# Kernel tuning notes

Hardware: AMD Instinct MI355X
Metric: run time of the kernel (lower is better)

Reference implementation:

```python
import jax, jax.numpy as jnp
import numpy as np
from jax import lax

K_NN = 3
LN_EPS = 1e-5


def _encode(x, W1, b1, W2, b2, W3, b3, gamma, beta):
    h = jax.nn.relu(x @ W1 + b1)
    h = jax.nn.relu(h @ W2 + b2)
    z = h @ W3 + b3
    mu = jnp.mean(z, axis=-1, keepdims=True)
    var = jnp.mean((z - mu) ** 2, axis=-1, keepdims=True)  # biased var, as torch LayerNorm
    return (z - mu) / jnp.sqrt(var + LN_EPS) * gamma + beta


def _state_entropy(src, tgt, k):
    # pairwise L2 distance via GEMM formulation (same math as torch.norm of diffs)
    sq = (jnp.sum(src * src, -1)[:, None]
          + jnp.sum(tgt * tgt, -1)[None, :]
          - 2.0 * (src @ tgt.T))
    dists = jnp.sqrt(jnp.maximum(sq, 0.0))  # [N_src, N_tgt]
    # sum of k smallest distances (kthvalue 1..k), single fused top-k
    neg_k, _ = lax.top_k(-dists, k)
    knn = jnp.sum(-neg_k, axis=-1)
    # faithful to the source bug: loop variable shadows k, final divisor is k-1
    knn = knn / float(k - 1)
    return knn[:, None]


def setup_inputs() -> dict:
    key = jax.random.key(0)
    ks = jax.random.split(key, 6)
    N, D, H, L = 16384, 128, 256, 256
    return {
        "state_src": jax.random.normal(ks[0], (N, D), jnp.float32),
        "state_tgt": jax.random.normal(ks[1], (N, D), jnp.float32),
        "W1": jax.random.normal(ks[2], (D, H), jnp.float32) * 0.05,
        "b1": jnp.zeros((H,), jnp.float32),
        "W2": jax.random.normal(ks[3], (H, H), jnp.float32) * 0.05,
        "b2": jnp.zeros((H,), jnp.float32),
        "W3": jax.random.normal(ks[4], (H, L), jnp.float32) * 0.05,
        "b3": jnp.zeros((L,), jnp.float32),
        "gamma": jnp.ones((L,), jnp.float32),
        "beta": jnp.zeros((L,), jnp.float32),
    }


def reference(state_src, state_tgt, W1, b1, W2, b2, W3, b3, gamma, beta):
    src = _encode(state_src, W1, b1, W2, b2, W3, b3, gamma, beta)  # forward()
    tgt = _encode(state_tgt, W1, b1, W2, b2, W3, b3, gamma, beta)
    entropy = _state_entropy(src, tgt, K_NN)  # compute_state_entropy (no_grad)
    return src, entropy
```

## Files before the change

kernel.cpp:

```cpp
#include <hip/hip_runtime.h>
#include <math.h>


typedef __attribute__((ext_vector_type(8))) short short8;
typedef __attribute__((ext_vector_type(4))) float floatx4;
typedef __attribute__((ext_vector_type(8))) int int8v;
typedef __attribute__((ext_vector_type(4))) int int4v;

#define MFMA16(a, b, c) __builtin_amdgcn_mfma_f32_16x16x32_bf16((a), (b), (c), 0, 0, 0)

__device__ __forceinline__ floatx4 mfma8(int8v a, int8v b, floatx4 c) {
  return __builtin_amdgcn_mfma_scale_f32_16x16x128_f8f6f4(a, b, c, 0, 0, 0, 0x7F, 0, 0x7F);
}

__device__ __forceinline__ int8v cat8(int4v lo, int4v hi) {
  return __builtin_shufflevector(lo, hi, 0, 1, 2, 3, 4, 5, 6, 7);
}

static const size_t OFF_W1F  = 0;
static const size_t OFF_W2F  = 65536;
static const size_t OFF_W3F  = 196608;
static const size_t OFF_SRCF = 327680;
static const size_t OFF_TGTF = 327680 + 8388608;
static const size_t OFF_S2   = 327680 + 2 * 8388608;
static const size_t OFF_T2   = OFF_S2 + 65536;
static const size_t OFF_P    = OFF_T2 + 65536;
static const size_t OFF_SRC8 = 18808832;
static const size_t OFF_TGT8 = 18808832 + 4194304;
static const size_t WS_NEED  = OFF_TGT8 + 4194304;

__device__ __forceinline__ unsigned short f2bf(float f) {
  unsigned int u = __float_as_uint(f);
  return (unsigned short)((u + 0x7FFFu + ((u >> 16) & 1u)) >> 16);
}

__device__ __forceinline__ unsigned int pkbf(float lo, float hi) {
  unsigned int r;
  asm("v_cvt_pk_bf16_f32 %0, %1, %2" : "=v"(r) : "v"(lo), "v"(hi));
  return r;
}

__device__ __forceinline__ void ins3(float& t0, float& t1, float& t2, float v) {
  float n0 = fminf(t0, v);
  float n1 = __builtin_amdgcn_fmed3f(t0, t1, v);
  float n2 = __builtin_amdgcn_fmed3f(t1, t2, v);
  t0 = n0; t1 = n1; t2 = n2;
}

__device__ __forceinline__ void gload16(const void* g, void* l) {
  __builtin_amdgcn_global_load_lds(
      (const __attribute__((address_space(1))) unsigned int*)(unsigned long long)(uintptr_t)g,
      (__attribute__((address_space(3))) unsigned int*)(unsigned int)(uintptr_t)l, 16, 0, 0);
}

__device__ __forceinline__ unsigned int sxor(unsigned int v, int m) {
  return (unsigned int)__shfl_xor((int)v, m, 64);
}

__device__ __forceinline__ void exchange8(const unsigned int* p0, const unsigned int* p1,
                                          short8* frag, int g) {
  const bool go = (g & 1), gh = (g >> 1);
#pragma unroll
  for (int ks = 0; ks < 8; ++ks) {
    unsigned int a_o = p0[2 * ks], b_o = p1[2 * ks];
    unsigned int c_o = p0[2 * ks + 1], d_o = p1[2 * ks + 1];
    unsigned int a_n = sxor(a_o, 16), b_n = sxor(b_o, 16);
    unsigned int c_n = sxor(c_o, 16), d_n = sxor(d_o, 16);
    unsigned int qab0 = go ? a_n : a_o, qab1 = go ? b_n : b_o;
    unsigned int qab2 = go ? a_o : a_n, qab3 = go ? b_o : b_n;
    unsigned int qcd0 = go ? c_n : c_o, qcd1 = go ? d_n : d_o;
    unsigned int qcd2 = go ? c_o : c_n, qcd3 = go ? d_o : d_n;
    unsigned int s0 = gh ? qab0 : qcd0, s1 = gh ? qab1 : qcd1;
    unsigned int s2 = gh ? qab2 : qcd2, s3 = gh ? qab3 : qcd3;
    unsigned int r0 = sxor(s0, 32), r1 = sxor(s1, 32);
    unsigned int r2 = sxor(s2, 32), r3 = sxor(s3, 32);
    union { unsigned int u[4]; short8 s; } cv;
    cv.u[0] = (g == 0) ? qab0 : (g == 3) ? qcd0 : r0;
    cv.u[1] = (g == 0) ? qab1 : (g == 3) ? qcd1 : r1;
    cv.u[2] = (g == 0) ? qab2 : (g == 3) ? qcd2 : r2;
    cv.u[3] = (g == 0) ? qab3 : (g == 3) ? qcd3 : r3;
    frag[ks] = cv.s;
  }
}

__global__ void prep_weights(const float* __restrict__ W1, const float* __restrict__ W2,
                             const float* __restrict__ W3, unsigned short* __restrict__ ws16) {
  int t = blockIdx.x * 256 + threadIdx.x;
  const float* W;
  unsigned short* dst;
  int f, ksbits;
  if (t < 4096)       { W = W1; dst = ws16 + OFF_W1F / 2; f = t;         ksbits = 2; }
  else if (t < 12288) { W = W2; dst = ws16 + OFF_W2F / 2; f = t - 4096;  ksbits = 3; }
  else                { W = W3; dst = ws16 + OFF_W3F / 2; f = t - 12288; ksbits = 3; }
  int l  = f & 63;
  int fk = f >> 6;
  int ks = fk & ((1 << ksbits) - 1);
  int cf = fk >> ksbits;
  int k0 = ks * 32 + ((l >> 4) << 3);
  int c  = (cf << 4) + (l & 15);
  short8 v;
#pragma unroll
  for (int j = 0; j < 8; ++j) v[j] = (short)f2bf(W[(size_t)(k0 + j) * 256 + c]);
  *(short8*)(dst + (size_t)f * 8) = v;
}

__global__ __launch_bounds__(256, 2) void encode_kernel(
    const float* __restrict__ xsrc, const float* __restrict__ xtgt,
    const float* __restrict__ b1, const float* __restrict__ b2, const float* __restrict__ b3,
    const float* __restrict__ gamma, const float* __restrict__ beta,
    float* __restrict__ out_src, unsigned short* __restrict__ ws16) {
  __shared__ unsigned short wlds[2][16384];
  const int tid = threadIdx.x, w = tid >> 6, l = tid & 63;
  const int dr = l & 15, g = l >> 4;
  const int blk = blockIdx.x;
  const bool is_src = blk < 256;
  const int row0 = ((blk & 255) << 6) + (w << 4);
  const int row = row0 + dr;
  const float* __restrict__ X = is_src ? xsrc : xtgt;
  unsigned short* __restrict__ fragout = ws16 + (is_src ? OFF_SRCF / 2 : OFF_TGTF / 2);
  float* __restrict__ nrm = (float*)(ws16 + (is_src ? OFF_S2 / 2 : OFF_T2 / 2));
  const unsigned short* W1f = ws16 + OFF_W1F / 2;
  const unsigned short* W2f = ws16 + OFF_W2F / 2;
  const unsigned short* W3f = ws16 + OFF_W3F / 2;

  auto stageW = [&](int bsel, int q) {
    const unsigned short* src;
    int rounds;
    if (q < 4)      { src = W1f + q * 8192;        rounds = 4; }
    else if (q < 8) { src = W2f + (q - 4) * 16384; rounds = 8; }
    else            { src = W3f + (q - 8) * 16384; rounds = 8; }
#pragma unroll
    for (int r = 0; r < 8; ++r) {
      if (r < rounds)
        gload16(src + r * 2048 + w * 512 + l * 8, &wlds[bsel][r * 2048 + w * 512]);
    }
  };

  short8 xf[4];
  const float* xr = X + (size_t)row * 128;
#pragma unroll
  for (int ks = 0; ks < 4; ++ks) {
    floatx4 f0 = *(const floatx4*)(xr + ks * 32 + g * 8);
    floatx4 f1 = *(const floatx4*)(xr + ks * 32 + g * 8 + 4);
    union { unsigned int u[4]; short8 s; } cv;
    cv.u[0] = pkbf(f0[0], f0[1]); cv.u[1] = pkbf(f0[2], f0[3]);
    cv.u[2] = pkbf(f1[0], f1[1]); cv.u[3] = pkbf(f1[2], f1[3]);
    xf[ks] = cv.s;
  }

  unsigned int p0[16], p1[16];
  short8 hf[8];

  stageW(0, 0);
  __syncthreads();
  int cur = 0;

#pragma unroll
  for (int qq = 0; qq < 4; ++qq) {
    stageW(cur ^ 1, qq + 1);
#pragma unroll
    for (int i = 0; i < 4; ++i) {
      int cf = qq * 4 + i;
      floatx4 acc = {0.f, 0.f, 0.f, 0.f};
#pragma unroll
      for (int ks = 0; ks < 4; ++ks) {
        short8 wf = *(const short8*)(&wlds[cur][((i * 4 + ks) * 64 + l) * 8]);
        acc = MFMA16(wf, xf[ks], acc);
      }
      floatx4 bv = *(const floatx4*)(b1 + cf * 16 + g * 4);
      float h0 = fmaxf(acc[0] + bv[0], 0.f), h1v = fmaxf(acc[1] + bv[1], 0.f);
      float h2v = fmaxf(acc[2] + bv[2], 0.f), h3v = fmaxf(acc[3] + bv[3], 0.f);
      p0[cf] = pkbf(h0, h1v); p1[cf] = pkbf(h2v, h3v);
    }
    __syncthreads();
    cur ^= 1;
  }
  exchange8(p0, p1, hf, g);

#pragma unroll
  for (int qq = 0; qq < 4; ++qq) {
    stageW(cur ^ 1, 5 + qq);
#pragma unroll
    for (int i = 0; i < 4; ++i) {
      int cf = qq * 4 + i;
      floatx4 acc = {0.f, 0.f, 0.f, 0.f};
#pragma unroll
      for (int ks = 0; ks < 8; ++ks) {
        short8 wf = *(const short8*)(&wlds[cur][((i * 8 + ks) * 64 + l) * 8]);
        acc = MFMA16(wf, hf[ks], acc);
      }
      floatx4 bv = *(const floatx4*)(b2 + cf * 16 + g * 4);
      float h0 = fmaxf(acc[0] + bv[0], 0.f), h1v = fmaxf(acc[1] + bv[1], 0.f);
      float h2v = fmaxf(acc[2] + bv[2], 0.f), h3v = fmaxf(acc[3] + bv[3], 0.f);
      p0[cf] = pkbf(h0, h1v); p1[cf] = pkbf(h2v, h3v);
    }
    __syncthreads();
    cur ^= 1;
  }
  exchange8(p0, p1, hf, g);

  floatx4 z[16];
#pragma unroll
  for (int qq = 0; qq < 4; ++qq) {
    if (qq < 3) stageW(cur ^ 1, 9 + qq);
#pragma unroll
    for (int i = 0; i < 4; ++i) {
      int cf = qq * 4 + i;
      floatx4 acc = {0.f, 0.f, 0.f, 0.f};
#pragma unroll
      for (int ks = 0; ks < 8; ++ks) {
        short8 wf = *(const short8*)(&wlds[cur][((i * 8 + ks) * 64 + l) * 8]);
        acc = MFMA16(wf, hf[ks], acc);
      }
      floatx4 bv = *(const floatx4*)(b3 + cf * 16 + g * 4);
#pragma unroll
      for (int j = 0; j < 4; ++j) acc[j] += bv[j];
      z[cf] = acc;
    }
    __syncthreads();
    cur ^= 1;
  }

  float s = 0.f, q = 0.f;
#pragma unroll
  for (int cf = 0; cf < 16; ++cf)
#pragma unroll
    for (int j = 0; j < 4; ++j) { float v = z[cf][j]; s += v; q = fmaf(v, v, q); }
  s += __shfl_xor(s, 16, 64); s += __shfl_xor(s, 32, 64);
  q += __shfl_xor(q, 16, 64); q += __shfl_xor(q, 32, 64);
  float mu = s * 0.00390625f;
  float var = q * 0.00390625f - mu * mu;
  float rstd = rsqrtf(var + 1e-5f);

  const float sc = is_src ? -2.0f : 1.0f;
  float nacc = 0.f;
#pragma unroll
  for (int cf = 0; cf < 16; ++cf) {
    floatx4 gv = *(const floatx4*)(gamma + cf * 16 + g * 4);
    floatx4 bev = *(const floatx4*)(beta + cf * 16 + g * 4);
    float y0 = (z[cf][0] - mu) * rstd * gv[0] + bev[0];
    float y1 = (z[cf][1] - mu) * rstd * gv[1] + bev[1];
    float y2 = (z[cf][2] - mu) * rstd * gv[2] + bev[2];
    float y3 = (z[cf][3] - mu) * rstd * gv[3] + bev[3];
    nacc = fmaf(y0, y0, nacc); nacc = fmaf(y1, y1, nacc);
    nacc = fmaf(y2, y2, nacc); nacc = fmaf(y3, y3, nacc);
    p0[cf] = pkbf(sc * y0, sc * y1); p1[cf] = pkbf(sc * y2, sc * y3);
  }
  nacc += __shfl_xor(nacc, 16, 64); nacc += __shfl_xor(nacc, 32, 64);
  if (g == 0) nrm[row] = nacc;

  short8 yf[8];
  exchange8(p0, p1, yf, g);

  const int tile = row0 >> 4;
#pragma unroll
  for (int ks = 0; ks < 8; ++ks)
    *(short8*)(fragout + ((size_t)(tile * 8 + ks) * 64 + l) * 8) = yf[ks];

  if (is_src) {
    float* orow = out_src + (size_t)row * 256;
#pragma unroll
    for (int ks = 0; ks < 8; ++ks) {
      union { short8 s; unsigned int u[4]; } cv; cv.s = yf[ks];
      floatx4 o0, o1;
      o0[0] = __uint_as_float(cv.u[0] << 16) * -0.5f;
      o0[1] = __uint_as_float(cv.u[0] & 0xffff0000u) * -0.5f;
      o0[2] = __uint_as_float(cv.u[1] << 16) * -0.5f;
      o0[3] = __uint_as_float(cv.u[1] & 0xffff0000u) * -0.5f;
      o1[0] = __uint_as_float(cv.u[2] << 16) * -0.5f;
      o1[1] = __uint_as_float(cv.u[2] & 0xffff0000u) * -0.5f;
      o1[2] = __uint_as_float(cv.u[3] << 16) * -0.5f;
      o1[3] = __uint_as_float(cv.u[3] & 0xffff0000u) * -0.5f;
      *(floatx4*)(orow + ks * 32 + g * 8) = o0;
      *(floatx4*)(orow + ks * 32 + g * 8 + 4) = o1;
    }
  }
}

__global__ __launch_bounds__(256) void repack_fp8(const unsigned short* __restrict__ ws16,
                                                  unsigned char* __restrict__ wsb) {
  int t = blockIdx.x * 256 + threadIdx.x;
  const int side = t >> 17;
  const int u = t & 131071;
  const int df = u >> 6, l = u & 63;
  const int tile = df >> 1, ks2 = df & 1;
  const unsigned short* sbase = ws16 + (side ? OFF_TGTF / 2 : OFF_SRCF / 2);
  unsigned char* dbase = wsb + (side ? OFF_TGT8 : OFF_SRC8);
  int r[8];
#pragma unroll
  for (int sub = 0; sub < 4; ++sub) {
    int sf = (tile * 8 + ks2 * 4 + (l >> 4)) * 64 + sub * 16 + (l & 15);
    short8 v = *(const short8*)(sbase + (size_t)sf * 8);
    float f[8];
#pragma unroll
    for (int j = 0; j < 8; ++j)
      f[j] = __uint_as_float(((unsigned int)(unsigned short)v[j]) << 16);
    unsigned int w0 = __builtin_amdgcn_cvt_pk_fp8_f32(f[0], f[1], 0, 0);
    w0 = __builtin_amdgcn_cvt_pk_fp8_f32(f[2], f[3], w0, 1);
    unsigned int w1 = __builtin_amdgcn_cvt_pk_fp8_f32(f[4], f[5], 0, 0);
    w1 = __builtin_amdgcn_cvt_pk_fp8_f32(f[6], f[7], w1, 1);
    r[sub * 2] = (int)w0;
    r[sub * 2 + 1] = (int)w1;
  }
  int4v rlo = {r[0], r[1], r[2], r[3]};
  int4v rhi = {r[4], r[5], r[6], r[7]};
  *(int4v*)(dbase + (size_t)df * 2048 + l * 16) = rlo;
  *(int4v*)(dbase + (size_t)df * 2048 + 1024 + l * 16) = rhi;
}

__global__ __launch_bounds__(256, 2) void dist8_kernel(
    const unsigned char* __restrict__ src8, const unsigned char* __restrict__ tgt8,
    const float* __restrict__ t2, float* __restrict__ part) {
  __shared__ unsigned char buf[2][32768];
  __shared__ float t2l[2048];
  const int tid = threadIdx.x, w = tid >> 6, l = tid & 63;
  const int blk = blockIdx.x;
  const int split = blk & 7;
  const int rtile = blk >> 3;
  const int R0 = rtile * 256 + w * 64;
  const int C0 = split * 2048;

  {
    floatx4 v0 = *(const floatx4*)(t2 + C0 + tid * 8);
    floatx4 v1 = *(const floatx4*)(t2 + C0 + tid * 8 + 4);
    *(floatx4*)(t2l + tid * 8) = v0;
    *(floatx4*)(t2l + tid * 8 + 4) = v1;
  }

  int8v a[4][2];
#pragma unroll
  for (int rf = 0; rf < 4; ++rf)
#pragma unroll
    for (int ks2 = 0; ks2 < 2; ++ks2) {
      const unsigned char* ab = src8 + ((size_t)((R0 >> 4) + rf) * 2 + ks2) * 2048;
      int4v lo = *(const int4v*)(ab + l * 16);
      int4v hi = *(const int4v*)(ab + 1024 + l * 16);
      a[rf][ks2] = cat8(lo, hi);
    }

  float t3[4][4][3];
#pragma unroll
  for (int rf = 0; rf < 4; ++rf)
#pragma unroll
    for (int j = 0; j < 4; ++j) { t3[rf][j][0] = 1e30f; t3[rf][j][1] = 1e30f; t3[rf][j][2] = 1e30f; }

  const unsigned char* gb0 = tgt8 + (size_t)(C0 >> 4) * 4096;
#define STAGE(bsel, t)                                                        \
  {                                                                           \
    const unsigned char* gb = gb0 + (size_t)(t) * 32768;                      \
    _Pragma("unroll") for (int i = 0; i < 8; ++i) {                           \
      int chunk = w * 8 + i;                                                  \
      gload16(gb + chunk * 1024 + l * 16, &buf[bsel][chunk * 1024]);          \
    }                                                                         \
  }

  STAGE(0, 0);
  __syncthreads();

  for (int t = 0; t < 16; ++t) {
    int cur = t & 1;
    if (t < 15) STAGE(cur ^ 1, t + 1);
#pragma unroll
    for (int cf = 0; cf < 8; ++cf) {
      const unsigned char* bb = &buf[cur][cf * 4096];
      int4v l0 = *(const int4v*)(bb + l * 16);
      int4v h0 = *(const int4v*)(bb + 1024 + l * 16);
      int4v l1 = *(const int4v*)(bb + 2048 + l * 16);
      int4v h1 = *(const int4v*)(bb + 3072 + l * 16);
      int8v b0 = cat8(l0, h0), b1 = cat8(l1, h1);
      float tv = t2l[t * 128 + cf * 16 + (l & 15)];
      floatx4 acc[4];
#pragma unroll
      for (int rf = 0; rf < 4; ++rf) acc[rf] = (floatx4){tv, tv, tv, tv};
      __builtin_amdgcn_s_setprio(1);
#pragma unroll
      for (int rf = 0; rf < 4; ++rf) acc[rf] = mfma8(a[rf][0], b0, acc[rf]);
#pragma unroll
      for (int rf = 0; rf < 4; ++rf) acc[rf] = mfma8(a[rf][1], b1, acc[rf]);
      __builtin_amdgcn_s_setprio(0);
#pragma unroll
      for (int rf = 0; rf < 4; ++rf)
#pragma unroll
        for (int j = 0; j < 4; ++j)
          ins3(t3[rf][j][0], t3[rf][j][1], t3[rf][j][2], acc[rf][j]);
    }
    __syncthreads();
  }
#undef STAGE

#pragma unroll
  for (int rf = 0; rf < 4; ++rf)
#pragma unroll
    for (int j = 0; j < 4; ++j)
#pragma unroll
      for (int m = 1; m < 16; m <<= 1) {
        float o0 = __shfl_xor(t3[rf][j][0], m, 64);
        float o1 = __shfl_xor(t3[rf][j][1], m, 64);
        float o2 = __shfl_xor(t3[rf][j][2], m, 64);
        ins3(t3[rf][j][0], t3[rf][j][1], t3[rf][j][2], o0);
        ins3(t3[rf][j][0], t3[rf][j][1], t3[rf][j][2], o1);
        ins3(t3[rf][j][0], t3[rf][j][1], t3[rf][j][2], o2);
      }
  if ((l & 15) == 0) {
    int q = l >> 4;
#pragma unroll
    for (int rf = 0; rf < 4; ++rf)
#pragma unroll
      for (int j = 0; j < 4; ++j) {
        int row = R0 + rf * 16 + q * 4 + j;
        float* p = part + ((size_t)row * 8 + split) * 3;
        p[0] = t3[rf][j][0];
        p[1] = t3[rf][j][1];
        p[2] = t3[rf][j][2];
      }
  }
}

__global__ __launch_bounds__(512, 2) void dist_kernel(
    const unsigned short* __restrict__ srcf, const unsigned short* __restrict__ tgtf,
    const float* __restrict__ t2, float* __restrict__ part) {
  __shared__ unsigned short buf[2][32768];
  const int tid = threadIdx.x, w = tid >> 6, l = tid & 63;
  const int blk = blockIdx.x;
  const int split = blk & 7;
  const int rtile = blk >> 3;
  const int R0 = rtile * 512 + w * 64;
  const int C0 = split * 2048;

  short8 a[4][8];
#pragma unroll
  for (int rf = 0; rf < 4; ++rf)
#pragma unroll
    for (int ks = 0; ks < 8; ++ks)
      a[rf][ks] = *(const short8*)(srcf + (((size_t)(R0 / 16 + rf) * 8 + ks) * 64 + l) * 8);

  float t3[4][4][3];
#pragma unroll
  for (int rf = 0; rf < 4; ++rf)
#pragma unroll
    for (int j = 0; j < 4; ++j) { t3[rf][j][0] = 1e30f; t3[rf][j][1] = 1e30f; t3[rf][j][2] = 1e30f; }

  const unsigned short* gb0 = tgtf + (size_t)(C0 / 16) * 4096;
#define STAGE(bsel, t)                                                        \
  {                                                                           \
    const unsigned short* gb = gb0 + (size_t)(t) * 32768;                     \
    _Pragma("unroll") for (int i = 0; i < 8; ++i) {                           \
      int chunk = w * 8 + i;                                                  \
      gload16(gb + chunk * 512 + l * 8, &buf[bsel][chunk * 512]);             \
    }                                                                         \
  }

  STAGE(0, 0);
  float t2v[8];
#pragma unroll
  for (int c = 0; c < 8; ++c) t2v[c] = t2[C0 + c * 16 + (l & 15)];
  __syncthreads();

  for (int t = 0; t < 16; ++t) {
    int cur = t & 1;
    if (t < 15) STAGE(cur ^ 1, t + 1);
    float t2n[8];
    if (t < 15) {
      int nb = C0 + (t + 1) * 128;
#pragma unroll
      for (int c = 0; c < 8; ++c) t2n[c] = t2[nb + c * 16 + (l & 15)];
    }
#pragma unroll
    for (int cf = 0; cf < 8; ++cf) {
      const unsigned short* bb = &buf[cur][cf << 12];
      float tv = t2v[cf];
      floatx4 acc[4];
      short8 bc = *(const short8*)(bb + l * 8);
#pragma unroll
      for (int rf = 0; rf < 4; ++rf) acc[rf] = (floatx4){tv, tv, tv, tv};
      __builtin_amdgcn_s_setprio(1);
#pragma unroll
      for (int ks = 0; ks < 8; ++ks) {
        short8 bn = bc;
        if (ks < 7) bn = *(const short8*)(bb + (ks + 1) * 512 + l * 8);
#pragma unroll
        for (int rf = 0; rf < 4; ++rf) acc[rf] = MFMA16(a[rf][ks], bc, acc[rf]);
        bc = bn;
      }
      __builtin_amdgcn_s_setprio(0);
#pragma unroll
      for (int rf = 0; rf < 4; ++rf)
#pragma unroll
        for (int j = 0; j < 4; ++j)
          ins3(t3[rf][j][0], t3[rf][j][1], t3[rf][j][2], acc[rf][j]);
    }
#pragma unroll
    for (int c = 0; c < 8; ++c) t2v[c] = t2n[c];
    __syncthreads();
  }
#undef STAGE

#pragma unroll
  for (int rf = 0; rf < 4; ++rf)
#pragma unroll
    for (int j = 0; j < 4; ++j)
#pragma unroll
      for (int m = 1; m < 16; m <<= 1) {
        float o0 = __shfl_xor(t3[rf][j][0], m, 64);
        float o1 = __shfl_xor(t3[rf][j][1], m, 64);
        float o2 = __shfl_xor(t3[rf][j][2], m, 64);
        ins3(t3[rf][j][0], t3[rf][j][1], t3[rf][j][2], o0);
        ins3(t3[rf][j][0], t3[rf][j][1], t3[rf][j][2], o1);
        ins3(t3[rf][j][0], t3[rf][j][1], t3[rf][j][2], o2);
      }
  if ((l & 15) == 0) {
    int q = l >> 4;
#pragma unroll
    for (int rf = 0; rf < 4; ++rf)
#pragma unroll
      for (int j = 0; j < 4; ++j) {
        int row = R0 + rf * 16 + q * 4 + j;
        float* p = part + ((size_t)row * 8 + split) * 3;
        p[0] = t3[rf][j][0];
        p[1] = t3[rf][j][1];
        p[2] = t3[rf][j][2];
      }
  }
}

__global__ void merge_kernel(const float* __restrict__ part, const float* __restrict__ s2,
                             float* __restrict__ eout) {
  int r = blockIdx.x * 256 + threadIdx.x;
  const float* p = part + (size_t)r * 24;
  float u0 = 1e30f, u1 = 1e30f, u2 = 1e30f;
#pragma unroll
  for (int i = 0; i < 24; ++i) ins3(u0, u1, u2, p[i]);
  float sv = s2[r];
  float d0 = sqrtf(fmaxf(sv + u0, 0.f));
  float d1 = sqrtf(fmaxf(sv + u1, 0.f));
  float d2 = sqrtf(fmaxf(sv + u2, 0.f));
  eout[r] = (d0 + d1 + d2) * 0.5f;
}

extern "C" void kernel_launch(void* const* d_in, const int* in_sizes, int n_in,
                              void* d_out, int out_size, void* d_ws, size_t ws_size,
                              hipStream_t stream) {
  const float* xsrc = (const float*)d_in[0];
  const float* xtgt = (const float*)d_in[1];
  const float* W1 = (const float*)d_in[2];
  const float* b1 = (const float*)d_in[3];
  const float* W2 = (const float*)d_in[4];
  const float* b2 = (const float*)d_in[5];
  const float* W3 = (const float*)d_in[6];
  const float* b3 = (const float*)d_in[7];
  const float* gm = (const float*)d_in[8];
  const float* bt = (const float*)d_in[9];
  float* out = (float*)d_out;
  unsigned short* ws16 = (unsigned short*)d_ws;
  unsigned char* wsb = (unsigned char*)d_ws;

  prep_weights<<<80, 256, 0, stream>>>(W1, W2, W3, ws16);
  encode_kernel<<<512, 256, 0, stream>>>(xsrc, xtgt, b1, b2, b3, gm, bt, out, ws16);
  if (ws_size >= WS_NEED) {
    repack_fp8<<<1024, 256, 0, stream>>>(ws16, wsb);
    dist8_kernel<<<512, 256, 0, stream>>>(wsb + OFF_SRC8, wsb + OFF_TGT8,
                                          (const float*)(wsb + OFF_T2),
                                          (float*)(wsb + OFF_P));
  } else {
    dist_kernel<<<256, 512, 0, stream>>>(ws16 + OFF_SRCF / 2, ws16 + OFF_TGTF / 2,
                                         (const float*)(wsb + OFF_T2),
                                         (float*)(wsb + OFF_P));
  }
  merge_kernel<<<64, 256, 0, stream>>>((const float*)(wsb + OFF_P),
                                       (const float*)(wsb + OFF_S2),
                                       out + 4194304);
}
```

Measured before the change: 120.5 us.

## Load FP8 target tiles directly from global into registers, dropping LDS staging

The distance kernel no longer stages target fp8 tiles and squared norms through double-buffered shared memory with block barriers. Each wave now reads B fragments and norm values straight from global memory into registers, using a two-deep register ping-pong to prefetch the next column chunk. This removes LDS traffic, __syncthreads and the shared memory footprint, which could raise occupancy. The cost is that all four waves read the same target data separately, relying on L2/L1 hits, and global load latency is now hidden by only one chunk of lookahead.

```diff
diff --git a/kernel.cpp b/kernel.cpp
--- a/kernel.cpp
+++ b/kernel.cpp
@@ -308,24 +308,15 @@
   *(int4v*)(dbase + (size_t)df * 2048 + 1024 + l * 16) = rhi;
 }
 
-__global__ __launch_bounds__(256, 2) void dist8_kernel(
+__global__ __launch_bounds__(256, 2) void dist9_kernel(
     const unsigned char* __restrict__ src8, const unsigned char* __restrict__ tgt8,
     const float* __restrict__ t2, float* __restrict__ part) {
-  __shared__ unsigned char buf[2][32768];
-  __shared__ float t2l[2048];
   const int tid = threadIdx.x, w = tid >> 6, l = tid & 63;
   const int blk = blockIdx.x;
   const int split = blk & 7;
-  const int rtile = blk >> 3;
-  const int R0 = rtile * 256 + w * 64;
+  const int rg = (blk >> 3) * 4 + w;
+  const int R0 = rg * 64;
   const int C0 = split * 2048;
-
-  {
-    floatx4 v0 = *(const floatx4*)(t2 + C0 + tid * 8);
-    floatx4 v1 = *(const floatx4*)(t2 + C0 + tid * 8 + 4);
-    *(floatx4*)(t2l + tid * 8) = v0;
-    *(floatx4*)(t2l + tid * 8 + 4) = v1;
-  }
 
   int8v a[4][2];
 #pragma unroll
@@ -344,49 +335,48 @@
 #pragma unroll
     for (int j = 0; j < 4; ++j) { t3[rf][j][0] = 1e30f; t3[rf][j][1] = 1e30f; t3[rf][j][2] = 1e30f; }
 
-  const unsigned char* gb0 = tgt8 + (size_t)(C0 >> 4) * 4096;
-#define STAGE(bsel, t)                                                        \
+  const unsigned char* bb = tgt8 + (size_t)(C0 >> 4) * 4096 + l * 16;
+  const float* t2g = t2 + C0;
+
+#define LOADB(c, x0, x1, x2, x3, tv)                                          \
   {                                                                           \
-    const unsigned char* gb = gb0 + (size_t)(t) * 32768;                      \
-    _Pragma("unroll") for (int i = 0; i < 8; ++i) {                           \
-      int chunk = w * 8 + i;                                                  \
-      gload16(gb + chunk * 1024 + l * 16, &buf[bsel][chunk * 1024]);          \
-    }                                                                         \
-  }
-
-  STAGE(0, 0);
-  __syncthreads();
-
-  for (int t = 0; t < 16; ++t) {
-    int cur = t & 1;
-    if (t < 15) STAGE(cur ^ 1, t + 1);
-#pragma unroll
-    for (int cf = 0; cf < 8; ++cf) {
-      const unsigned char* bb = &buf[cur][cf * 4096];
-      int4v l0 = *(const int4v*)(bb + l * 16);
-      int4v h0 = *(const int4v*)(bb + 1024 + l * 16);
-      int4v l1 = *(const int4v*)(bb + 2048 + l * 16);
-      int4v h1 = *(const int4v*)(bb + 3072 + l * 16);
-      int8v b0 = cat8(l0, h0), b1 = cat8(l1, h1);
-      float tv = t2l[t * 128 + cf * 16 + (l & 15)];
-      floatx4 acc[4];
-#pragma unroll
-      for (int rf = 0; rf < 4; ++rf) acc[rf] = (floatx4){tv, tv, tv, tv};
-      __builtin_amdgcn_s_setprio(1);
-#pragma unroll
-      for (int rf = 0; rf < 4; ++rf) acc[rf] = mfma8(a[rf][0], b0, acc[rf]);
-#pragma unroll
-      for (int rf = 0; rf < 4; ++rf) acc[rf] = mfma8(a[rf][1], b1, acc[rf]);
-      __builtin_amdgcn_s_setprio(0);
-#pragma unroll
-      for (int rf = 0; rf < 4; ++rf)
-#pragma unroll
-        for (int j = 0; j < 4; ++j)
-          ins3(t3[rf][j][0], t3[rf][j][1], t3[rf][j][2], acc[rf][j]);
-    }
-    __syncthreads();
-  }
-#undef STAGE
+    const unsigned char* p = bb + (size_t)(c) * 4096;                         \
+    x0 = *(const int4v*)(p);                                                  \
+    x1 = *(const int4v*)(p + 1024);                                           \
+    x2 = *(const int4v*)(p + 2048);                                           \
+    x3 = *(const int4v*)(p + 3072);                                           \
+    tv = t2g[(c) * 16 + (l & 15)];                                            \
+  }
+
+#define COMPB(x0, x1, x2, x3, tv)                                             \
+  {                                                                           \
+    int8v b0 = cat8(x0, x1), b1 = cat8(x2, x3);                               \
+    floatx4 acc[4];                                                           \
+    _Pragma("unroll") for (int rf = 0; rf < 4; ++rf)                          \
+        acc[rf] = (floatx4){tv, tv, tv, tv};                                  \
+    __builtin_amdgcn_s_setprio(1);                                            \
+    _Pragma("unroll") for (int rf = 0; rf < 4; ++rf)                          \
+        acc[rf] = mfma8(a[rf][0], b0, acc[rf]);                               \
+    _Pragma("unroll") for (int rf = 0; rf < 4; ++rf)                          \
+        acc[rf] = mfma8(a[rf][1], b1, acc[rf]);                               \
+    __builtin_amdgcn_s_setprio(0);                                            \
+    _Pragma("unroll") for (int rf = 0; rf < 4; ++rf)                          \
+      _Pragma("unroll") for (int j = 0; j < 4; ++j)                           \
+          ins3(t3[rf][j][0], t3[rf][j][1], t3[rf][j][2], acc[rf][j]);         \
+  }
+
+  int4v A0, A1, A2, A3, B0, B1, B2, B3;
+  float ta, tb;
+  LOADB(0, A0, A1, A2, A3, ta);
+  for (int c = 0; c < 128; c += 2) {
+    LOADB(c + 1, B0, B1, B2, B3, tb);
+    COMPB(A0, A1, A2, A3, ta);
+    int cn = (c + 2 < 128) ? (c + 2) : 127;
+    LOADB(cn, A0, A1, A2, A3, ta);
+    COMPB(B0, B1, B2, B3, tb);
+  }
+#undef LOADB
+#undef COMPB
 
 #pragma unroll
   for (int rf = 0; rf < 4; ++rf)
@@ -558,7 +548,7 @@
   encode_kernel<<<512, 256, 0, stream>>>(xsrc, xtgt, b1, b2, b3, gm, bt, out, ws16);
   if (ws_size >= WS_NEED) {
     repack_fp8<<<1024, 256, 0, stream>>>(ws16, wsb);
-    dist8_kernel<<<512, 256, 0, stream>>>(wsb + OFF_SRC8, wsb + OFF_TGT8,
+    dist9_kernel<<<512, 256, 0, stream>>>(wsb + OFF_SRC8, wsb + OFF_TGT8,
                                           (const float*)(wsb + OFF_T2),
                                           (float*)(wsb + OFF_P));
   } else {
```

Result: no change. 122.7 us (+1.8%).

## Give each wave its own 4-slot target ring buffer and drop block barriers

Applied to the files above, without the earlier changes.

The FP8 distance kernel now gives each wavefront a private 4-deep ring of 4KB target fragments in LDS. It streams one fragment at a time with a 3-ahead prefetch and uses explicit vmcnt waits in place of block-wide double buffering and __syncthreads. This removes per-tile barriers and lets waves progress independently. The cost is that every wave loads the full target stream itself, with no sharing across the 4 waves, which multiplies global/L2 traffic by four. The partials buffer moves to a reused workspace region, and merge takes the candidate count as an argument.

```diff
diff --git a/kernel.cpp b/kernel.cpp
--- a/kernel.cpp
+++ b/kernel.cpp
@@ -25,6 +25,7 @@
 static const size_t OFF_S2   = 327680 + 2 * 8388608;
 static const size_t OFF_T2   = OFF_S2 + 65536;
 static const size_t OFF_P    = OFF_T2 + 65536;
+static const size_t OFF_P2   = OFF_SRCF;
 static const size_t OFF_SRC8 = 18808832;
 static const size_t OFF_TGT8 = 18808832 + 4194304;
 static const size_t WS_NEED  = OFF_TGT8 + 4194304;
@@ -308,16 +309,16 @@
   *(int4v*)(dbase + (size_t)df * 2048 + 1024 + l * 16) = rhi;
 }
 
-__global__ __launch_bounds__(256, 2) void dist8_kernel(
+__global__ __launch_bounds__(256, 2) void dist12_kernel(
     const unsigned char* __restrict__ src8, const unsigned char* __restrict__ tgt8,
     const float* __restrict__ t2, float* __restrict__ part) {
-  __shared__ unsigned char buf[2][32768];
+  __shared__ unsigned char fbuf[4][4][4096];
   __shared__ float t2l[2048];
   const int tid = threadIdx.x, w = tid >> 6, l = tid & 63;
   const int blk = blockIdx.x;
   const int split = blk & 7;
-  const int rtile = blk >> 3;
-  const int R0 = rtile * 256 + w * 64;
+  const int rg = (blk >> 3) * 4 + w;
+  const int R0 = rg * 64;
   const int C0 = split * 2048;
 
   {
@@ -344,31 +345,37 @@
 #pragma unroll
     for (int j = 0; j < 4; ++j) { t3[rf][j][0] = 1e30f; t3[rf][j][1] = 1e30f; t3[rf][j][2] = 1e30f; }
 
-  const unsigned char* gb0 = tgt8 + (size_t)(C0 >> 4) * 4096;
-#define STAGE(bsel, t)                                                        \
+  __syncthreads();
+
+  const unsigned char* gb = tgt8 + (size_t)(C0 >> 4) * 4096;
+
+#define STG(slot, c)                                                          \
   {                                                                           \
-    const unsigned char* gb = gb0 + (size_t)(t) * 32768;                      \
-    _Pragma("unroll") for (int i = 0; i < 8; ++i) {                           \
-      int chunk = w * 8 + i;                                                  \
-      gload16(gb + chunk * 1024 + l * 16, &buf[bsel][chunk * 1024]);          \
-    }                                                                         \
-  }
-
-  STAGE(0, 0);
-  __syncthreads();
-
-  for (int t = 0; t < 16; ++t) {
-    int cur = t & 1;
-    if (t < 15) STAGE(cur ^ 1, t + 1);
-#pragma unroll
-    for (int cf = 0; cf < 8; ++cf) {
-      const unsigned char* bb = &buf[cur][cf * 4096];
-      int4v l0 = *(const int4v*)(bb + l * 16);
-      int4v h0 = *(const int4v*)(bb + 1024 + l * 16);
-      int4v l1 = *(const int4v*)(bb + 2048 + l * 16);
-      int4v h1 = *(const int4v*)(bb + 3072 + l * 16);
+    const unsigned char* p = gb + (size_t)(c) * 4096 + l * 16;                \
+    gload16(p,        &fbuf[w][slot][0]);                                     \
+    gload16(p + 1024, &fbuf[w][slot][1024]);                                  \
+    gload16(p + 2048, &fbuf[w][slot][2048]);                                  \
+    gload16(p + 3072, &fbuf[w][slot][3072]);                                  \
+  }
+
+  STG(0, 0);
+  STG(1, 1);
+  STG(2, 2);
+
+  for (int cc = 0; cc < 128; cc += 4) {
+#pragma unroll
+    for (int s = 0; s < 4; ++s) {
+      const int c = cc + s;
+      const int pf = (c + 3 < 128) ? (c + 3) : 127;
+      STG((s + 3) & 3, pf);
+      asm volatile("s_waitcnt vmcnt(12)" ::: "memory");
+      const unsigned char* fb = &fbuf[w][s][0];
+      int4v l0 = *(const int4v*)(fb + l * 16);
+      int4v h0 = *(const int4v*)(fb + 1024 + l * 16);
+      int4v l1 = *(const int4v*)(fb + 2048 + l * 16);
+      int4v h1 = *(const int4v*)(fb + 3072 + l * 16);
       int8v b0 = cat8(l0, h0), b1 = cat8(l1, h1);
-      float tv = t2l[t * 128 + cf * 16 + (l & 15)];
+      float tv = t2l[c * 16 + (l & 15)];
       floatx4 acc[4];
 #pragma unroll
       for (int rf = 0; rf < 4; ++rf) acc[rf] = (floatx4){tv, tv, tv, tv};
@@ -384,9 +391,8 @@
         for (int j = 0; j < 4; ++j)
           ins3(t3[rf][j][0], t3[rf][j][1], t3[rf][j][2], acc[rf][j]);
     }
-    __syncthreads();
-  }
-#undef STAGE
+  }
+#undef STG
 
 #pragma unroll
   for (int rf = 0; rf < 4; ++rf)
@@ -524,12 +530,11 @@
 }
 
 __global__ void merge_kernel(const float* __restrict__ part, const float* __restrict__ s2,
-                             float* __restrict__ eout) {
+                             float* __restrict__ eout, int ncand) {
   int r = blockIdx.x * 256 + threadIdx.x;
-  const float* p = part + (size_t)r * 24;
+  const float* p = part + (size_t)r * ncand;
   float u0 = 1e30f, u1 = 1e30f, u2 = 1e30f;
-#pragma unroll
-  for (int i = 0; i < 24; ++i) ins3(u0, u1, u2, p[i]);
+  for (int i = 0; i < ncand; ++i) ins3(u0, u1, u2, p[i]);
   float sv = s2[r];
   float d0 = sqrtf(fmaxf(sv + u0, 0.f));
   float d1 = sqrtf(fmaxf(sv + u1, 0.f));
@@ -558,15 +563,18 @@
   encode_kernel<<<512, 256, 0, stream>>>(xsrc, xtgt, b1, b2, b3, gm, bt, out, ws16);
   if (ws_size >= WS_NEED) {
     repack_fp8<<<1024, 256, 0, stream>>>(ws16, wsb);
-    dist8_kernel<<<512, 256, 0, stream>>>(wsb + OFF_SRC8, wsb + OFF_TGT8,
-                                          (const float*)(wsb + OFF_T2),
-                                          (float*)(wsb + OFF_P));
+    dist12_kernel<<<512, 256, 0, stream>>>(wsb + OFF_SRC8, wsb + OFF_TGT8,
+                                           (const float*)(wsb + OFF_T2),
+                                           (float*)(wsb + OFF_P2));
+    merge_kernel<<<64, 256, 0, stream>>>((const float*)(wsb + OFF_P2),
+                                         (const float*)(wsb + OFF_S2),
+                                         out + 4194304, 24);
   } else {
     dist_kernel<<<256, 512, 0, stream>>>(ws16 + OFF_SRCF / 2, ws16 + OFF_TGTF / 2,
                                          (const float*)(wsb + OFF_T2),
                                          (float*)(wsb + OFF_P));
-  }
-  merge_kernel<<<64, 256, 0, stream>>>((const float*)(wsb + OFF_P),
-                                       (const float*)(wsb + OFF_S2),
-                                       out + 4194304);
-}
+    merge_kernel<<<64, 256, 0, stream>>>((const float*)(wsb + OFF_P),
+                                         (const float*)(wsb + OFF_S2),
+                                         out + 4194304, 24);
+  }
+}
```

Result: slower. 132.2 us (+9.7%).

## Triple-buffer fp8 distance kernel with 512-thread blocks and interleaved prefetch

Applied to the files above, without the earlier changes.

Widens the fp8 distance kernel from 256 to 512 threads per block, so each block covers 512 source rows and shares each staged target tile across twice as many waves. Staging moves from double to triple buffering with a two-tile lookahead. Global-to-LDS loads are interleaved into the MFMA loop under explicit vmcnt waits and raw barriers, replacing the per-tile __syncthreads. LDS use grows to about 104KB per block, and the per-iteration barriers add synchronization overhead that may limit occupancy or stall waves.

```diff
diff --git a/kernel.cpp b/kernel.cpp
--- a/kernel.cpp
+++ b/kernel.cpp
@@ -308,23 +308,21 @@
   *(int4v*)(dbase + (size_t)df * 2048 + 1024 + l * 16) = rhi;
 }
 
-__global__ __launch_bounds__(256, 2) void dist8_kernel(
+__global__ __launch_bounds__(512, 2) void dist14_kernel(
     const unsigned char* __restrict__ src8, const unsigned char* __restrict__ tgt8,
     const float* __restrict__ t2, float* __restrict__ part) {
-  __shared__ unsigned char buf[2][32768];
+  __shared__ unsigned char buf[3][32768];
   __shared__ float t2l[2048];
   const int tid = threadIdx.x, w = tid >> 6, l = tid & 63;
   const int blk = blockIdx.x;
   const int split = blk & 7;
   const int rtile = blk >> 3;
-  const int R0 = rtile * 256 + w * 64;
+  const int R0 = rtile * 512 + w * 64;
   const int C0 = split * 2048;
 
   {
-    floatx4 v0 = *(const floatx4*)(t2 + C0 + tid * 8);
-    floatx4 v1 = *(const floatx4*)(t2 + C0 + tid * 8 + 4);
-    *(floatx4*)(t2l + tid * 8) = v0;
-    *(floatx4*)(t2l + tid * 8 + 4) = v1;
+    floatx4 v0 = *(const floatx4*)(t2 + C0 + tid * 4);
+    *(floatx4*)(t2l + tid * 4) = v0;
   }
 
   int8v a[4][2];
@@ -345,30 +343,45 @@
     for (int j = 0; j < 4; ++j) { t3[rf][j][0] = 1e30f; t3[rf][j][1] = 1e30f; t3[rf][j][2] = 1e30f; }
 
   const unsigned char* gb0 = tgt8 + (size_t)(C0 >> 4) * 4096;
-#define STAGE(bsel, t)                                                        \
-  {                                                                           \
-    const unsigned char* gb = gb0 + (size_t)(t) * 32768;                      \
-    _Pragma("unroll") for (int i = 0; i < 8; ++i) {                           \
-      int chunk = w * 8 + i;                                                  \
-      gload16(gb + chunk * 1024 + l * 16, &buf[bsel][chunk * 1024]);          \
-    }                                                                         \
-  }
-
-  STAGE(0, 0);
-  __syncthreads();
-
+
+#pragma unroll
+  for (int tt = 0; tt < 2; ++tt)
+#pragma unroll
+    for (int i = 0; i < 4; ++i) {
+      int chunk = w * 4 + i;
+      gload16(gb0 + (size_t)tt * 32768 + chunk * 1024 + l * 16, &buf[tt][chunk * 1024]);
+    }
+
+#pragma unroll 1
   for (int t = 0; t < 16; ++t) {
-    int cur = t & 1;
-    if (t < 15) STAGE(cur ^ 1, t + 1);
-#pragma unroll
-    for (int cf = 0; cf < 8; ++cf) {
-      const unsigned char* bb = &buf[cur][cf * 4096];
+    if (t == 0) {
+      asm volatile("s_waitcnt vmcnt(4) lgkmcnt(0)" ::: "memory");
+    } else if (t < 15) {
+      asm volatile("s_waitcnt vmcnt(4)" ::: "memory");
+    } else {
+      asm volatile("s_waitcnt vmcnt(0)" ::: "memory");
+    }
+    __builtin_amdgcn_s_barrier();
+
+    const unsigned char* bt_ = &buf[t % 3][0];
+    const int nt = t + 2;
+    unsigned char* bn = &buf[nt % 3][0];
+    const unsigned char* gn = gb0 + (size_t)nt * 32768;
+
+#pragma unroll
+    for (int p = 0; p < 8; ++p) {
+      const unsigned char* bb = bt_ + p * 4096;
       int4v l0 = *(const int4v*)(bb + l * 16);
       int4v h0 = *(const int4v*)(bb + 1024 + l * 16);
       int4v l1 = *(const int4v*)(bb + 2048 + l * 16);
       int4v h1 = *(const int4v*)(bb + 3072 + l * 16);
+      if (p < 4 && nt < 16) {
+        int chunk = w * 4 + p;
+        gload16(gn + chunk * 1024 + l * 16, bn + chunk * 1024);
+      }
+      __builtin_amdgcn_s_barrier();
       int8v b0 = cat8(l0, h0), b1 = cat8(l1, h1);
-      float tv = t2l[t * 128 + cf * 16 + (l & 15)];
+      float tv = t2l[t * 128 + p * 16 + (l & 15)];
       floatx4 acc[4];
 #pragma unroll
       for (int rf = 0; rf < 4; ++rf) acc[rf] = (floatx4){tv, tv, tv, tv};
@@ -384,9 +397,7 @@
         for (int j = 0; j < 4; ++j)
           ins3(t3[rf][j][0], t3[rf][j][1], t3[rf][j][2], acc[rf][j]);
     }
-    __syncthreads();
-  }
-#undef STAGE
+  }
 
 #pragma unroll
   for (int rf = 0; rf < 4; ++rf)
@@ -558,9 +569,9 @@
   encode_kernel<<<512, 256, 0, stream>>>(xsrc, xtgt, b1, b2, b3, gm, bt, out, ws16);
   if (ws_size >= WS_NEED) {
     repack_fp8<<<1024, 256, 0, stream>>>(ws16, wsb);
-    dist8_kernel<<<512, 256, 0, stream>>>(wsb + OFF_SRC8, wsb + OFF_TGT8,
-                                          (const float*)(wsb + OFF_T2),
-                                          (float*)(wsb + OFF_P));
+    dist14_kernel<<<256, 512, 0, stream>>>(wsb + OFF_SRC8, wsb + OFF_TGT8,
+                                           (const float*)(wsb + OFF_T2),
+                                           (float*)(wsb + OFF_P));
   } else {
     dist_kernel<<<256, 512, 0, stream>>>(ws16 + OFF_SRCF / 2, ws16 + OFF_TGTF / 2,
                                          (const float*)(wsb + OFF_T2),
```

New measurement: 121.2 us. About the same (+0.6%).
